# Kernel tuning notes

Hardware: AMD Instinct MI355X
Metric: run time of the kernel (lower is better)

Reference implementation:

```python
import jax, jax.numpy as jnp
import numpy as np
from jax import lax

KEEP_PROB = 0.9
BLOCK_SIZE = 7


def setup_inputs() -> dict:
    key = jax.random.key(0)
    x = jax.random.normal(key, (64, 64, 112, 112), dtype=jnp.float32)
    return {"x": x}


def _block_mask(init_mask, k):
    # Faithful vectorized form of the nested-loop dilation:
    # original zeroes out[i-k : i+k, j-k : j+k) (exclusive upper bound) around
    # every zero in init_mask, i.e. out[a,b] = min over i in [a-k+1, a+k],
    # j in [b-k+1, b+k] of init_mask -> min-pool (erosion) with window 2k,
    # asymmetric padding (k-1, k). Padding with init value 1.0 is the identity
    # for min on a {0,1} mask.
    return lax.reduce_window(
        init_mask,
        jnp.array(1.0, init_mask.dtype),
        lax.min,
        window_dimensions=(1, 2 * k, 2 * k),
        window_strides=(1, 1, 1),
        padding=((0, 0), (k - 1, k), (k - 1, k)),
    )


def reference(x):
    B, C, H, W = x.shape
    bs = BLOCK_SIZE
    # gamma = (1-keep_prob) * H^2 / (bs^2 * (H-bs+1)^2)
    gamma = (1.0 - KEEP_PROB) * (H ** 2) / (bs ** 2 * (H - bs + 1) ** 2)
    key = jax.random.key(42)
    # bernoulli(1-gamma): 1 = keep, 0 = drop-center
    init_mask = jax.random.bernoulli(key, 1.0 - gamma, (B, H, W)).astype(x.dtype)
    mask = _block_mask(init_mask, bs // 2)  # [B, H, W]
    out = x * mask[:, None, :, :]
    # renormalize: * (B*H*W) / sum(out)  (matches original, sums over all elems)
    out = out * (B * H * W) / jnp.sum(out)
    return out
```

## Files before the change

### kernel.cpp

```cpp
#include <hip/hip_runtime.h>
#include <stdint.h>

#define B_      64
#define C_      64
#define H_      112
#define W_      112
#define HW_     12544
#define HW4_    3136
#define CHW4_   200704
#define NPART   1024

typedef float v4f __attribute__((ext_vector_type(4)));

__device__ __forceinline__ uint32_t rotl32(uint32_t x, int d) {
  return (x << d) | (x >> (32 - d));
}

__device__ __forceinline__ uint32_t threefry_bits(uint32_t i) {
  const uint32_t k0 = 0u, k1 = 42u;
  const uint32_t k2 = k0 ^ k1 ^ 0x1BD11BDAu;
  uint32_t x0 = 0u, x1 = i;
  x0 += k0; x1 += k1;
#define TF_R(r) { x0 += x1; x1 = rotl32(x1, (r)); x1 ^= x0; }
  TF_R(13) TF_R(15) TF_R(26) TF_R(6)
  x0 += k1; x1 += k2 + 1u;
  TF_R(17) TF_R(29) TF_R(16) TF_R(24)
  x0 += k2; x1 += k0 + 2u;
  TF_R(13) TF_R(15) TF_R(26) TF_R(6)
  x0 += k0; x1 += k1 + 3u;
  TF_R(17) TF_R(29) TF_R(16) TF_R(24)
  x0 += k1; x1 += k2 + 4u;
  TF_R(13) TF_R(15) TF_R(26) TF_R(6)
  x0 += k2; x1 += k0 + 5u;
#undef TF_R
  return x0 ^ x1;
}

__global__ __launch_bounds__(256) void k_mask(uint8_t* __restrict__ mask,
                                              float p) {
  __shared__ uint8_t t0[9 * W_];
  __shared__ uint8_t t1[4 * W_];
  const int b = blockIdx.y;
  const int r0 = blockIdx.x << 2;
  const int tid = threadIdx.x;
  for (int i = tid; i < 9 * W_; i += 256) {
    int row = i / W_;
    int j = i - row * W_;
    int r = r0 - 2 + row;
    uint8_t v = 1;
    if (r >= 0 && r < H_) {
      uint32_t bits = threefry_bits((uint32_t)(b * HW_ + r * W_ + j));
      float u = __uint_as_float((bits >> 9) | 0x3f800000u) - 1.0f;
      v = (u < p) ? (uint8_t)1 : (uint8_t)0;
    }
    t0[i] = v;
  }
  __syncthreads();
  for (int i = tid; i < 4 * W_; i += 256) {
    int row = i / W_;
    int j = i - row * W_;
    unsigned v = t0[row * W_ + j];
    v &= t0[(row + 1) * W_ + j];
    v &= t0[(row + 2) * W_ + j];
    v &= t0[(row + 3) * W_ + j];
    v &= t0[(row + 4) * W_ + j];
    v &= t0[(row + 5) * W_ + j];
    t1[i] = (uint8_t)v;
  }
  __syncthreads();
  for (int i = tid; i < 4 * W_; i += 256) {
    int row = i / W_;
    int j = i - row * W_;
    int lo = j - 2; if (lo < 0) lo = 0;
    int hi = j + 3; if (hi > W_ - 1) hi = W_ - 1;
    unsigned v = 1u;
    for (int jj = lo; jj <= hi; ++jj) v &= t1[row * W_ + jj];
    mask[b * HW_ + (r0 + row) * W_ + j] = (uint8_t)v;
  }
}

__global__ __launch_bounds__(256) void k_sum(const float4* __restrict__ x4,
                                             const uint8_t* __restrict__ mask,
                                             float* __restrict__ partials) {
  const int b = blockIdx.y;
  const int cg = blockIdx.x;
  const float4* xp = x4 + (size_t)b * CHW4_ + (size_t)(cg * 4) * HW4_;
  const uint32_t* m32 = (const uint32_t*)(mask + b * HW_);
  float acc = 0.0f;
  for (int c = 0; c < 4; ++c) {
    const float4* xc = xp + (size_t)c * HW4_;
#pragma unroll 4
    for (int hw4 = threadIdx.x; hw4 < HW4_; hw4 += 256) {
      uint32_t mw = m32[hw4];
      float4 v = xc[hw4];
      acc += (mw & 0x000000ffu) ? v.x : 0.0f;
      acc += (mw & 0x0000ff00u) ? v.y : 0.0f;
      acc += (mw & 0x00ff0000u) ? v.z : 0.0f;
      acc += (mw & 0xff000000u) ? v.w : 0.0f;
    }
  }
  for (int off = 32; off > 0; off >>= 1)
    acc += __shfl_down(acc, off, 64);
  __shared__ float part[4];
  if ((threadIdx.x & 63) == 0) part[threadIdx.x >> 6] = acc;
  __syncthreads();
  if (threadIdx.x == 0)
    partials[b * 16 + cg] = part[0] + part[1] + part[2] + part[3];
}

__global__ __launch_bounds__(256) void k_scale(const float4* __restrict__ x4,
                                               const uint8_t* __restrict__ mask,
                                               const float* __restrict__ partials,
                                               v4f* __restrict__ out4) {
  __shared__ float sscale;
  {
    double a = 0.0;
    for (int i = threadIdx.x; i < NPART; i += 256)
      a += (double)partials[i];
    for (int off = 32; off > 0; off >>= 1)
      a += __shfl_down(a, off, 64);
    __shared__ double dp[4];
    if ((threadIdx.x & 63) == 0) dp[threadIdx.x >> 6] = a;
    __syncthreads();
    if (threadIdx.x == 0) {
      double s = dp[0] + dp[1] + dp[2] + dp[3];
      sscale = (float)(802816.0 / s);
    }
    __syncthreads();
  }
  const float scale = sscale;
  const int b = blockIdx.y;
  const size_t base = (size_t)b * CHW4_ + (size_t)blockIdx.x * HW4_;
  const float4* xp = x4 + base;
  v4f* op = out4 + base;
  const uint32_t* m32 = (const uint32_t*)(mask + b * HW_);
  for (int hw4 = threadIdx.x; hw4 < HW4_; hw4 += 256) {
    uint32_t mw = m32[hw4];
    float4 v = xp[hw4];
    v4f o;
    o.x = (mw & 0x000000ffu) ? v.x * scale : 0.0f;
    o.y = (mw & 0x0000ff00u) ? v.y * scale : 0.0f;
    o.z = (mw & 0x00ff0000u) ? v.z * scale : 0.0f;
    o.w = (mw & 0xff000000u) ? v.w * scale : 0.0f;
    __builtin_nontemporal_store(o, &op[hw4]);
  }
}

extern "C" void kernel_launch(void* const* d_in, const int* in_sizes, int n_in,
                              void* d_out, int out_size, void* d_ws, size_t ws_size,
                              hipStream_t stream) {
  const float* x = (const float*)d_in[0];
  float* out = (float*)d_out;
  char* ws = (char*)d_ws;
  float* partials = (float*)(ws + 16);
  uint8_t* mask = (uint8_t*)(ws + 16384);

  double gamma = (1.0 - 0.9) * 12544.0 / 550564.0;
  float p = (float)(1.0 - gamma);

  k_mask <<<dim3(28, 64), 256, 0, stream>>>(mask, p);
  k_sum  <<<dim3(16, 64), 256, 0, stream>>>((const float4*)x, mask, partials);
  k_scale<<<dim3(64, 64), 256, 0, stream>>>((const float4*)x, mask, partials,
                                            (v4f*)out);
}
```

Before: 383.4 us.

## Fuse mask generation with masked partial sum over 4-row slabs

Merges the mask kernel and the masked-sum kernel into one. Each block builds its 4-row mask slab in shared memory, then reads x for that row slab across all 64 channels and sums it, giving 1792 partials. This removes a kernel launch and the global re-read of the mask, and overlaps the RNG compute with x loads. In exchange, each block's x reads become strided 1792-byte row slabs per channel instead of contiguous planes, and the partials reduction grows.

```diff
diff --git a/kernel.cpp b/kernel.cpp
--- a/kernel.cpp
+++ b/kernel.cpp
@@ -8,7 +8,8 @@
 #define HW_     12544
 #define HW4_    3136
 #define CHW4_   200704
-#define NPART   1024
+#define NPART   1792
+#define SLABF4  7168
 
 typedef float v4f __attribute__((ext_vector_type(4)));
 
@@ -36,13 +37,17 @@
   return x0 ^ x1;
 }
 
-__global__ __launch_bounds__(256) void k_mask(uint8_t* __restrict__ mask,
-                                              float p) {
+__global__ __launch_bounds__(256) void k_masksum(
+    const float4* __restrict__ x4, uint8_t* __restrict__ mask,
+    float* __restrict__ partials, float p) {
   __shared__ uint8_t t0[9 * W_];
   __shared__ uint8_t t1[4 * W_];
+  __shared__ uint32_t m2w[4 * 28];
   const int b = blockIdx.y;
-  const int r0 = blockIdx.x << 2;
+  const int rc = blockIdx.x;
+  const int r0 = rc << 2;
   const int tid = threadIdx.x;
+
   for (int i = tid; i < 9 * W_; i += 256) {
     int row = i / W_;
     int j = i - row * W_;
@@ -75,37 +80,31 @@
     int hi = j + 3; if (hi > W_ - 1) hi = W_ - 1;
     unsigned v = 1u;
     for (int jj = lo; jj <= hi; ++jj) v &= t1[row * W_ + jj];
+    ((uint8_t*)m2w)[i] = (uint8_t)v;
     mask[b * HW_ + (r0 + row) * W_ + j] = (uint8_t)v;
   }
-}
+  __syncthreads();
 
-__global__ __launch_bounds__(256) void k_sum(const float4* __restrict__ x4,
-                                             const uint8_t* __restrict__ mask,
-                                             float* __restrict__ partials) {
-  const int b = blockIdx.y;
-  const int cg = blockIdx.x;
-  const float4* xp = x4 + (size_t)b * CHW4_ + (size_t)(cg * 4) * HW4_;
-  const uint32_t* m32 = (const uint32_t*)(mask + b * HW_);
+  const float4* xb = x4 + (size_t)b * CHW4_ + rc * 112;
   float acc = 0.0f;
-  for (int c = 0; c < 4; ++c) {
-    const float4* xc = xp + (size_t)c * HW4_;
 #pragma unroll 4
-    for (int hw4 = threadIdx.x; hw4 < HW4_; hw4 += 256) {
-      uint32_t mw = m32[hw4];
-      float4 v = xc[hw4];
-      acc += (mw & 0x000000ffu) ? v.x : 0.0f;
-      acc += (mw & 0x0000ff00u) ? v.y : 0.0f;
-      acc += (mw & 0x00ff0000u) ? v.z : 0.0f;
-      acc += (mw & 0xff000000u) ? v.w : 0.0f;
-    }
+  for (int f = tid; f < SLABF4; f += 256) {
+    unsigned c = (unsigned)f / 112u;
+    unsigned s = (unsigned)f - c * 112u;
+    float4 v = xb[c * 3136u + s];
+    uint32_t mw = m2w[s];
+    acc += (mw & 0x000000ffu) ? v.x : 0.0f;
+    acc += (mw & 0x0000ff00u) ? v.y : 0.0f;
+    acc += (mw & 0x00ff0000u) ? v.z : 0.0f;
+    acc += (mw & 0xff000000u) ? v.w : 0.0f;
   }
   for (int off = 32; off > 0; off >>= 1)
     acc += __shfl_down(acc, off, 64);
   __shared__ float part[4];
-  if ((threadIdx.x & 63) == 0) part[threadIdx.x >> 6] = acc;
+  if ((tid & 63) == 0) part[tid >> 6] = acc;
   __syncthreads();
-  if (threadIdx.x == 0)
-    partials[b * 16 + cg] = part[0] + part[1] + part[2] + part[3];
+  if (tid == 0)
+    partials[b * 28 + rc] = part[0] + part[1] + part[2] + part[3];
 }
 
 __global__ __launch_bounds__(256) void k_scale(const float4* __restrict__ x4,
@@ -158,8 +157,8 @@
   double gamma = (1.0 - 0.9) * 12544.0 / 550564.0;
   float p = (float)(1.0 - gamma);
 
-  k_mask <<<dim3(28, 64), 256, 0, stream>>>(mask, p);
-  k_sum  <<<dim3(16, 64), 256, 0, stream>>>((const float4*)x, mask, partials);
-  k_scale<<<dim3(64, 64), 256, 0, stream>>>((const float4*)x, mask, partials,
-                                            (v4f*)out);
+  k_masksum<<<dim3(28, 64), 256, 0, stream>>>((const float4*)x, mask,
+                                              partials, p);
+  k_scale  <<<dim3(64, 64), 256, 0, stream>>>((const float4*)x, mask,
+                                              partials, (v4f*)out);
 }
```

New measurement: 374.1 us. 2.4% less time.
